# Optimization experiments

Measured on AMD Instinct MI355X. Metric: run time of the kernel, lower is better.

The kernel has to match this reference:

```python
import jax, jax.numpy as jnp
import numpy as np

B, S, D, H = 4, 2048, 256, 4
HD = D // H          # head_dim = 64
SPARSITY = 0.1
NH2 = H * H          # 16, distill feature size


def _linear_params(key, out_d, in_d):
    # torch nn.Linear default init: U(-1/sqrt(in), 1/sqrt(in)) for W and b
    limit = 1.0 / np.sqrt(in_d)
    kw, kb = jax.random.split(key)
    W = jax.random.uniform(kw, (out_d, in_d), minval=-limit, maxval=limit, dtype=jnp.float32)
    b = jax.random.uniform(kb, (out_d,), minval=-limit, maxval=limit, dtype=jnp.float32)
    return W, b


def setup_inputs() -> dict:
    key = jax.random.key(0)
    ks = jax.random.split(key, 8)
    x = jax.random.normal(ks[0], (B, S, D), dtype=jnp.float32)
    Wq, bq = _linear_params(ks[1], D, D)
    Wk, bk = _linear_params(ks[2], D, D)
    Wv, bv = _linear_params(ks[3], D, D)
    Wd, bd = _linear_params(ks[4], NH2, NH2)      # distill: 16 -> 16
    Wg, bg = _linear_params(ks[5], NH2, D)        # gate: dim -> 16 (then sigmoid)
    Wgp, bgp = _linear_params(ks[6], D, NH2)      # gate_projection: 16 -> dim
    Wo, bo = _linear_params(ks[7], D, D)          # out: dim -> dim
    return dict(x=x, Wq=Wq, bq=bq, Wk=Wk, bk=bk, Wv=Wv, bv=bv,
                Wd=Wd, bd=bd, Wg=Wg, bg=bg, Wgp=Wgp, bgp=bgp, Wo=Wo, bo=bo)


def reference(x, Wq, bq, Wk, bk, Wv, bv, Wd, bd, Wg, bg, Wgp, bgp, Wo, bo):
    b, s, d = x.shape
    scale = HD ** -0.5
    # QKV projections, split into heads: [b, h, s, hd]
    Q = (x @ Wq.T + bq).reshape(b, s, H, HD).transpose(0, 2, 1, 3)
    K = (x @ Wk.T + bk).reshape(b, s, H, HD).transpose(0, 2, 1, 3)
    V = (x @ Wv.T + bv).reshape(b, s, H, HD).transpose(0, 2, 1, 3)
    scores = jnp.einsum('bhqd,bhkd->bhqk', Q, K) * scale  # [b,h,s,s]
    # per-row quantile threshold (torch.quantile linear interpolation == jnp default)
    q = 1.0 - SPARSITY  # 0.9
    thr = jnp.quantile(scores, q, axis=-1, keepdims=True)
    masked = jnp.where(scores >= thr, scores, -jnp.inf)
    probs = jax.nn.softmax(masked, axis=-1)
    att = jnp.einsum('bhqk,bhkd->bhqd', probs, V)
    att = att.transpose(0, 2, 1, 3).reshape(b, s, d)  # [b,s,dim]
    # distill: view as (-1, 16) -> Linear(16,16) -> view back
    distilled = (att.reshape(-1, NH2) @ Wd.T + bd).reshape(b, s, d)
    # gate from mean-pooled input
    g = jax.nn.sigmoid(x.mean(axis=1) @ Wg.T + bg)  # [b,16]
    g = (g @ Wgp.T + bgp)[:, None, :]               # [b,1,dim] broadcast over seq
    mixed = g * distilled + (1.0 - g) * att
    return mixed @ Wo.T + bo
```

## Files before the change

kernel.cpp:

```cpp
#include <hip/hip_runtime.h>
#include <hip/hip_bf16.h>
#include <math.h>


#define CAP 256

typedef __attribute__((ext_vector_type(8))) short short8;
typedef __attribute__((ext_vector_type(4))) float floatx4;
typedef _Float16 half8 __attribute__((ext_vector_type(8)));
typedef _Float16 half4v __attribute__((ext_vector_type(4)));
#define MFMA16(a,b,c) __builtin_amdgcn_mfma_f32_16x16x32_bf16(a,b,c,0,0,0)
#define MFMAH(a,b,c)  __builtin_amdgcn_mfma_f32_16x16x32_f16(a,b,c,0,0,0)

__device__ __forceinline__ float umt(unsigned u){
  return __uint_as_float((u & 0x80000000u) ? (u & 0x7fffffffu) : ~u);
}
__device__ __forceinline__ float wsum_f(float v){
  #pragma unroll
  for (int m=1;m<64;m<<=1) v += __shfl_xor(v,m,64);
  return v;
}
__device__ __forceinline__ float wmax_f(float v){
  #pragma unroll
  for (int m=1;m<64;m<<=1) v = fmaxf(v, __shfl_xor(v,m,64));
  return v;
}
__device__ __forceinline__ float wmin_f(float v){
  #pragma unroll
  for (int m=1;m<64;m<<=1) v = fminf(v, __shfl_xor(v,m,64));
  return v;
}
__device__ __forceinline__ int mbcnt64(unsigned long long m){
  return (int)__builtin_amdgcn_mbcnt_hi((unsigned)(m>>32),
         __builtin_amdgcn_mbcnt_lo((unsigned)(m & 0xffffffffull), 0u));
}
__device__ __forceinline__ short8 ldb8(const __hip_bfloat16* p){
  return *(const short8*)p;
}

__global__ void xpart_kernel(const float* __restrict__ x, float* __restrict__ xpart){
  const int ch = blockIdx.x, b = blockIdx.y, t = threadIdx.x;
  const float* xp = x + ((size_t)b*2048 + (size_t)ch*128)*256 + t;
  float s = 0.f;
  for (int i=0;i<128;i++) s += xp[(size_t)i*256];
  xpart[(size_t)(b*16+ch)*256 + t] = s;
}

__global__ void gate_kernel(const float* __restrict__ xpart,
                            const float* __restrict__ Wg, const float* __restrict__ bg,
                            const float* __restrict__ Wgp,const float* __restrict__ bgp,
                            float* __restrict__ gate_ws){
  __shared__ float xm[256];
  __shared__ float g16[16];
  const int t = threadIdx.x;
  for (int b=0;b<4;b++){
    float s = 0.f;
    for (int ch=0; ch<16; ch++) s += xpart[(size_t)(b*16+ch)*256 + t];
    xm[t] = s * (1.0f/2048.0f);
    __syncthreads();
    if (t < 16){
      float z = bg[t];
      for (int d=0; d<256; d++) z = fmaf(xm[d], Wg[t*256+d], z);
      g16[t] = 1.0f/(1.0f + __expf(-z));
    }
    __syncthreads();
    float z2 = bgp[t];
    #pragma unroll
    for (int j=0;j<16;j++) z2 = fmaf(g16[j], Wgp[t*16+j], z2);
    gate_ws[b*256 + t] = z2;
    __syncthreads();
  }
}

__global__ __launch_bounds__(256) void qkv_gemm(
    const float* __restrict__ x,
    const float* __restrict__ Wq, const float* __restrict__ bq,
    const float* __restrict__ Wk, const float* __restrict__ bk,
    const float* __restrict__ Wv, const float* __restrict__ bv,
    __hip_bfloat16* __restrict__ qh, __hip_bfloat16* __restrict__ ql,
    __hip_bfloat16* __restrict__ kh, __hip_bfloat16* __restrict__ kl,
    _Float16* __restrict__ vth, _Float16* __restrict__ vtl){
  __shared__ float As[16][68];
  __shared__ float Bs[16][68];
  const int m0 = blockIdx.x * 64;
  const int n0g = blockIdx.y * 64;
  const int sect = n0g >> 8;
  const int nloc0 = n0g & 255;
  const float* W    = (sect==0) ? Wq : ((sect==1) ? Wk : Wv);
  const float* bias = (sect==0) ? bq : ((sect==1) ? bk : bv);
  const int tid = threadIdx.x;
  const int ty = tid >> 4, tx = tid & 15;
  const int lr = tid >> 2, lc = tid & 3;

  float c[4][4];
  #pragma unroll
  for (int i=0;i<4;i++){
    #pragma unroll
    for (int j=0;j<4;j++) c[i][j]=0.f;
  }

  for (int k0=0; k0<256; k0+=16){
    float4 av  = *(const float4*)&x[(size_t)(m0+lr)*256 + k0 + lc*4];
    float4 bv4 = *(const float4*)&W[(size_t)(nloc0+lr)*256 + k0 + lc*4];
    __syncthreads();
    As[lc*4+0][lr]=av.x;  As[lc*4+1][lr]=av.y;  As[lc*4+2][lr]=av.z;  As[lc*4+3][lr]=av.w;
    Bs[lc*4+0][lr]=bv4.x; Bs[lc*4+1][lr]=bv4.y; Bs[lc*4+2][lr]=bv4.z; Bs[lc*4+3][lr]=bv4.w;
    __syncthreads();
    #pragma unroll
    for (int kk=0; kk<16; kk++){
      float4 a  = *(const float4*)&As[kk][ty*4];
      float4 b4 = *(const float4*)&Bs[kk][tx*4];
      c[0][0]=fmaf(a.x,b4.x,c[0][0]); c[0][1]=fmaf(a.x,b4.y,c[0][1]); c[0][2]=fmaf(a.x,b4.z,c[0][2]); c[0][3]=fmaf(a.x,b4.w,c[0][3]);
      c[1][0]=fmaf(a.y,b4.x,c[1][0]); c[1][1]=fmaf(a.y,b4.y,c[1][1]); c[1][2]=fmaf(a.y,b4.z,c[1][2]); c[1][3]=fmaf(a.y,b4.w,c[1][3]);
      c[2][0]=fmaf(a.z,b4.x,c[2][0]); c[2][1]=fmaf(a.z,b4.y,c[2][1]); c[2][2]=fmaf(a.z,b4.z,c[2][2]); c[2][3]=fmaf(a.z,b4.w,c[2][3]);
      c[3][0]=fmaf(a.w,b4.x,c[3][0]); c[3][1]=fmaf(a.w,b4.y,c[3][1]); c[3][2]=fmaf(a.w,b4.z,c[3][2]); c[3][3]=fmaf(a.w,b4.w,c[3][3]);
    }
  }

  if (sect == 2){
    const int mB = m0 + ty*4;
    const int bidx = mB >> 11, s0 = mB & 2047;
    #pragma unroll
    for (int j=0;j<4;j++){
      const int f = nloc0 + tx*4 + j;
      const int hh = f >> 6, hd = f & 63;
      const float bf = bias[f];
      half4v hv, lv;
      #pragma unroll
      for (int i=0;i<4;i++){
        const float val = c[i][j] + bf;
        const _Float16 hx = (_Float16)val;
        hv[i] = hx;
        lv[i] = (_Float16)(val - (float)hx);
      }
      const size_t row = (size_t)((bidx*4+hh)*64 + hd);
      *(half4v*)(vth + row*2048 + s0) = hv;
      *(half4v*)(vtl + row*2048 + s0) = lv;
    }
  } else {
    #pragma unroll
    for (int i=0;i<4;i++){
      const int m = m0 + ty*4 + i;
      const int bidx = m >> 11, s = m & 2047;
      #pragma unroll
      for (int j=0;j<4;j++){
        const int f = nloc0 + tx*4 + j;
        const float val = c[i][j] + bias[f];
        const int hh = f >> 6, hd = f & 63;
        const size_t idx = (size_t)((bidx*4+hh)*2048 + s)*64 + hd;
        const __hip_bfloat16 hi = __float2bfloat16(val);
        const float lo = val - __bfloat162float(hi);
        if (sect == 0){ qh[idx] = hi; ql[idx] = __float2bfloat16(lo); }
        else          { kh[idx] = hi; kl[idx] = __float2bfloat16(lo); }
      }
    }
  }
}

__global__ __launch_bounds__(512, 4) void attn_kernel(
    const __hip_bfloat16* __restrict__ qh, const __hip_bfloat16* __restrict__ ql,
    const __hip_bfloat16* __restrict__ kh, const __hip_bfloat16* __restrict__ kl,
    const _Float16* __restrict__ vth, const _Float16* __restrict__ vtl,
    float* __restrict__ att_ws){
  __shared__ __align__(16) char smem[74240];
  __shared__ float obuf[16][66];
  __shared__ float zbuf[16];

  float (*buf0)[516] = (float (*)[516])smem;
  float (*buf1)[516] = (float (*)[516])(smem + 33024);

  const int bh = blockIdx.y;
  const int q0 = blockIdx.x * 16;
  const int tid = threadIdx.x;
  const int w = tid >> 6, ln = tid & 63;
  const int lm = ln & 15;
  const int lk = (ln >> 4) * 8;
  const int qa = 2*w, qb = 2*w + 1;

  const __hip_bfloat16* Qh = qh + ((size_t)bh*2048 + q0)*64;
  const __hip_bfloat16* Ql = ql + ((size_t)bh*2048 + q0)*64;
  const __hip_bfloat16* Kh = kh + ((size_t)bh*2048 + w*256)*64;
  const __hip_bfloat16* Kl = kl + ((size_t)bh*2048 + w*256)*64;

  float su0[32], su1[32];

  const short8 ah0 = ldb8(Qh + lm*64 + lk);
  const short8 ah1 = ldb8(Qh + lm*64 + 32 + lk);
  const short8 al0 = ldb8(Ql + lm*64 + lk);
  const short8 al1 = ldb8(Ql + lm*64 + 32 + lk);

  #pragma unroll
  for (int c = 0; c < 4; c++){
    float (*bufc)[516] = (c & 1) ? buf1 : buf0;
    floatx4 acc[4];
    #pragma unroll
    for (int tl = 0; tl < 4; tl++){
      const int krow = c*64 + tl*16 + lm;
      short8 bh0 = ldb8(Kh + krow*64 + lk);
      short8 bh1 = ldb8(Kh + krow*64 + 32 + lk);
      short8 bl0 = ldb8(Kl + krow*64 + lk);
      short8 bl1 = ldb8(Kl + krow*64 + 32 + lk);
      floatx4 a = {0.f,0.f,0.f,0.f};
      a = MFMA16(ah0, bh0, a);
      a = MFMA16(ah1, bh1, a);
      a = MFMA16(al0, bh0, a);
      a = MFMA16(al1, bh1, a);
      a = MFMA16(ah0, bl0, a);
      a = MFMA16(ah1, bl1, a);
      a = MFMA16(al0, bl0, a);
      a = MFMA16(al1, bl1, a);
      acc[tl] = a;
    }
    const int wr = (ln >> 4) * 4;
    #pragma unroll
    for (int tl = 0; tl < 4; tl++){
      const int col = w*64 + tl*16 + lm;
      bufc[wr+0][col] = acc[tl].x * 0.125f;
      bufc[wr+1][col] = acc[tl].y * 0.125f;
      bufc[wr+2][col] = acc[tl].z * 0.125f;
      bufc[wr+3][col] = acc[tl].w * 0.125f;
    }
    __syncthreads();
    float4 ra0 = *(const float4*)&bufc[qa][4*ln];
    float4 ra1 = *(const float4*)&bufc[qa][256 + 4*ln];
    float4 rb0 = *(const float4*)&bufc[qb][4*ln];
    float4 rb1 = *(const float4*)&bufc[qb][256 + 4*ln];
    const int o = c*8;
    su0[o+0]=ra0.x; su0[o+1]=ra0.y; su0[o+2]=ra0.z; su0[o+3]=ra0.w;
    su0[o+4]=ra1.x; su0[o+5]=ra1.y; su0[o+6]=ra1.z; su0[o+7]=ra1.w;
    su1[o+0]=rb0.x; su1[o+1]=rb0.y; su1[o+2]=rb0.z; su1[o+3]=rb0.w;
    su1[o+4]=rb1.x; su1[o+5]=rb1.y; su1[o+6]=rb1.z; su1[o+7]=rb1.w;
  }
  __syncthreads();

  unsigned p0 = 0, p1 = 0;
  #pragma unroll 1
  for (int bit = 31; bit >= 20; --bit){
    const float c0f = umt(p0 | (1u << bit));
    const float c1f = umt(p1 | (1u << bit));
    int n0 = 0, n1 = 0;
    #pragma unroll
    for (int i = 0; i < 32; i++){
      n0 += (int)__popcll(__ballot(su0[i] >= c0f));
      n1 += (int)__popcll(__ballot(su1[i] >= c1f));
    }
    if (n0 >= 206) p0 |= (1u << bit);
    if (n1 >= 206) p1 |= (1u << bit);
  }

  const int b = bh >> 2, h = bh & 3;

  #pragma unroll
  for (int rr = 0; rr < 2; rr++){
    const int q = 2*w + rr;
    const unsigned p = rr ? p1 : p0;
    const float pf  = umt(p);
    const float hif = umt(p + 0x100000u);
    float* candw = (float*)(smem + 66048 + (size_t)w*1024);

    int above = 0, nc = 0;
    float mx = -3.0e38f;
    #pragma unroll
    for (int i = 0; i < 32; i++){
      const float u = rr ? su1[i] : su0[i];
      mx = fmaxf(mx, u);
      const bool ab = (u >= hif);
      const bool cd = (u >= pf) && !ab;
      above += (int)__popcll(__ballot(ab));
      const unsigned long long bal = __ballot(cd);
      if (cd){
        const int pos = nc + mbcnt64(bal);
        if (pos < CAP) candw[pos] = u;
      }
      nc += (int)__popcll(bal);
    }
    mx = wmax_f(mx);

    unsigned v;
    if (nc <= CAP){
      const int j = 206 - above;
      const float cv0 = (ln       < nc) ? candw[ln]       : -3.0e38f;
      const float cv1 = (ln + 64  < nc) ? candw[ln + 64]  : -3.0e38f;
      const float cv2 = (ln + 128 < nc) ? candw[ln + 128] : -3.0e38f;
      const float cv3 = (ln + 192 < nc) ? candw[ln + 192] : -3.0e38f;
      v = p;
      #pragma unroll 1
      for (int bit = 19; bit >= 0; --bit){
        const float cf = umt(v | (1u << bit));
        int n = (int)__popcll(__ballot(cv0 >= cf))
              + (int)__popcll(__ballot(cv1 >= cf))
              + (int)__popcll(__ballot(cv2 >= cf))
              + (int)__popcll(__ballot(cv3 >= cf));
        if (n >= j) v |= (1u << bit);
      }
    } else {
      v = p;
      #pragma unroll 1
      for (int bit = 19; bit >= 0; --bit){
        const float cf = umt(v | (1u << bit));
        int n = 0;
        #pragma unroll
        for (int i = 0; i < 32; i++)
          n += (int)__popcll(__ballot((rr ? su1[i] : su0[i]) >= cf));
        if (n >= 206) v |= (1u << bit);
      }
    }
    const float v206 = umt(v);

    int cgt = 0; float mn = 3.0e38f;
    #pragma unroll
    for (int i = 0; i < 32; i++){
      const float u = rr ? su1[i] : su0[i];
      const bool gt = (u > v206);
      cgt += (int)__popcll(__ballot(gt));
      mn = (gt && u < mn) ? u : mn;
    }
    mn = wmin_f(mn);
    const float v205 = (cgt == 205) ? mn : v206;

    const float thr = (float)((double)v206 + 0.3*((double)v205 - (double)v206));

    float zl = 0.f;
    char* rowbase = smem + (size_t)q*4096 + ((size_t)(ln >> 4) << 9)
                  + (size_t)((((ln & 15) << 3)) ^ ((q & 7) << 4));
    #pragma unroll
    for (int c = 0; c < 4; c++){
      #pragma unroll
      for (int h4 = 0; h4 < 2; h4++){
        half4v pk;
        #pragma unroll
        for (int jj = 0; jj < 4; jj++){
          const int i = c*8 + h4*4 + jj;
          const float s = rr ? su1[i] : su0[i];
          const float pr = (s >= thr) ? __expf(s - mx) : 0.f;
          const _Float16 ph = (_Float16)pr;
          zl += (float)ph;
          pk[jj] = ph;
        }
        *(half4v*)(rowbase + h4*2048 + c*128) = pk;
      }
    }
    const float Z = wsum_f(zl);
    if (ln == 0) zbuf[q] = 1.0f / Z;
  }

  __syncthreads();

  const int ct = w & 3, kh2 = w >> 2;
  const int arow = ln & 15;
  const int sw = (arow & 7) << 4;
  const char* prow = smem + (size_t)arow*4096;
  const int klog0 = (kh2 << 11) + ((ln >> 4) << 4);
  const _Float16* vhp = vth + ((size_t)bh*64 + ct*16 + arow)*2048 + (kh2 << 10) + ((ln >> 4) << 3);
  const _Float16* vlp = vtl + ((size_t)bh*64 + ct*16 + arow)*2048 + (kh2 << 10) + ((ln >> 4) << 3);

  floatx4 acch = {0.f,0.f,0.f,0.f};
  floatx4 accl = {0.f,0.f,0.f,0.f};
  #pragma unroll 4
  for (int kk = 0; kk < 32; kk++){
    const half8 a   = *(const half8*)(prow + ((klog0 + kk*64) ^ sw));
    const half8 vh8 = *(const half8*)(vhp + kk*32);
    const half8 vl8 = *(const half8*)(vlp + kk*32);
    acch = MFMAH(a, vh8, acch);
    accl = MFMAH(a, vl8, accl);
  }
  floatx4 acc = acch + accl;

  if (kh2 == 1){
    const int r0 = (ln >> 4) * 4;
    #pragma unroll
    for (int i = 0; i < 4; i++) obuf[r0+i][ct*16 + arow] = acc[i];
  }
  __syncthreads();
  if (kh2 == 0){
    const int r0 = (ln >> 4) * 4;
    #pragma unroll
    for (int i = 0; i < 4; i++){
      const int r = r0 + i;
      const float o = (acc[i] + obuf[r][ct*16 + arow]) * zbuf[r];
      att_ws[(size_t)(b*2048 + q0 + r)*256 + h*64 + ct*16 + arow] = o;
    }
  }
}

__global__ void mix_kernel(const float* __restrict__ att,
                           const float* __restrict__ Wd, const float* __restrict__ bd,
                           const float* __restrict__ gate, float* __restrict__ mix){
  __shared__ float wd_s[256];
  __shared__ float bd_s[16];
  const int tid = threadIdx.x;
  wd_s[tid] = Wd[tid];
  if (tid < 16) bd_s[tid] = bd[tid];
  __syncthreads();
  const int m = blockIdx.x*16 + (tid >> 4);
  const int j = tid & 15;
  const int b = m >> 11;
  const float* arow = att + (size_t)m*256;
  float* mrow = mix + (size_t)m*256;
  for (int g=0; g<16; g++){
    float d = bd_s[j];
    #pragma unroll
    for (int mm=0; mm<16; mm++) d = fmaf(arow[g*16+mm], wd_s[j*16+mm], d);
    const int cidx = g*16 + j;
    const float gt = gate[b*256 + cidx];
    mrow[cidx] = gt*d + (1.0f - gt)*arow[cidx];
  }
}

__global__ __launch_bounds__(256) void out_gemm(
    const float* __restrict__ A, const float* __restrict__ Wo,
    const float* __restrict__ bo, float* __restrict__ out){
  __shared__ float As[16][68];
  __shared__ float Bs[16][68];
  const int m0 = blockIdx.x * 64;
  const int n0 = blockIdx.y * 64;
  const int tid = threadIdx.x;
  const int ty = tid >> 4, tx = tid & 15;
  const int lr = tid >> 2, lc = tid & 3;

  float c[4][4];
  #pragma unroll
  for (int i=0;i<4;i++){
    #pragma unroll
    for (int j=0;j<4;j++) c[i][j]=0.f;
  }

  for (int k0=0; k0<256; k0+=16){
    float4 av  = *(const float4*)&A[(size_t)(m0+lr)*256 + k0 + lc*4];
    float4 bv4 = *(const float4*)&Wo[(size_t)(n0+lr)*256 + k0 + lc*4];
    __syncthreads();
    As[lc*4+0][lr]=av.x;  As[lc*4+1][lr]=av.y;  As[lc*4+2][lr]=av.z;  As[lc*4+3][lr]=av.w;
    Bs[lc*4+0][lr]=bv4.x; Bs[lc*4+1][lr]=bv4.y; Bs[lc*4+2][lr]=bv4.z; Bs[lc*4+3][lr]=bv4.w;
    __syncthreads();
    #pragma unroll
    for (int kk=0; kk<16; kk++){
      float4 a  = *(const float4*)&As[kk][ty*4];
      float4 b4 = *(const float4*)&Bs[kk][tx*4];
      c[0][0]=fmaf(a.x,b4.x,c[0][0]); c[0][1]=fmaf(a.x,b4.y,c[0][1]); c[0][2]=fmaf(a.x,b4.z,c[0][2]); c[0][3]=fmaf(a.x,b4.w,c[0][3]);
      c[1][0]=fmaf(a.y,b4.x,c[1][0]); c[1][1]=fmaf(a.y,b4.y,c[1][1]); c[1][2]=fmaf(a.y,b4.z,c[1][2]); c[1][3]=fmaf(a.y,b4.w,c[1][3]);
      c[2][0]=fmaf(a.z,b4.x,c[2][0]); c[2][1]=fmaf(a.z,b4.y,c[2][1]); c[2][2]=fmaf(a.z,b4.z,c[2][2]); c[2][3]=fmaf(a.z,b4.w,c[2][3]);
      c[3][0]=fmaf(a.w,b4.x,c[3][0]); c[3][1]=fmaf(a.w,b4.y,c[3][1]); c[3][2]=fmaf(a.w,b4.z,c[3][2]); c[3][3]=fmaf(a.w,b4.w,c[3][3]);
    }
  }
  #pragma unroll
  for (int i=0;i<4;i++){
    const int m = m0 + ty*4 + i;
    float4 st = make_float4(c[i][0]+bo[n0+tx*4+0], c[i][1]+bo[n0+tx*4+1],
                            c[i][2]+bo[n0+tx*4+2], c[i][3]+bo[n0+tx*4+3]);
    *(float4*)&out[(size_t)m*256 + n0 + tx*4] = st;
  }
}

extern "C" void kernel_launch(void* const* d_in, const int* in_sizes, int n_in,
                              void* d_out, int out_size, void* d_ws, size_t ws_size,
                              hipStream_t stream) {
  const float* x   = (const float*)d_in[0];
  const float* Wq  = (const float*)d_in[1];  const float* bq  = (const float*)d_in[2];
  const float* Wk  = (const float*)d_in[3];  const float* bk  = (const float*)d_in[4];
  const float* Wv  = (const float*)d_in[5];  const float* bv  = (const float*)d_in[6];
  const float* Wd  = (const float*)d_in[7];  const float* bd  = (const float*)d_in[8];
  const float* Wg  = (const float*)d_in[9];  const float* bg  = (const float*)d_in[10];
  const float* Wgp = (const float*)d_in[11]; const float* bgp = (const float*)d_in[12];
  const float* Wo  = (const float*)d_in[13]; const float* bo  = (const float*)d_in[14];

  char* base = (char*)d_ws;
  float* att_ws = (float*)(base);
  float* mix_ws = (float*)(base + (size_t)( 8<<20));
  __hip_bfloat16* qh = (__hip_bfloat16*)(base + (size_t)(16<<20));
  __hip_bfloat16* ql = (__hip_bfloat16*)(base + (size_t)(20<<20));
  __hip_bfloat16* kh = (__hip_bfloat16*)(base + (size_t)(24<<20));
  __hip_bfloat16* kl = (__hip_bfloat16*)(base + (size_t)(28<<20));
  _Float16* vth = (_Float16*)(base + (size_t)(32<<20));
  _Float16* vtl = (_Float16*)(base + (size_t)(36<<20));
  float* xpart  = (float*)(base + (size_t)(40<<20));
  float* gate_ws= (float*)(base + (size_t)(40<<20) + 65536);

  xpart_kernel<<<dim3(16,4), 256, 0, stream>>>(x, xpart);
  gate_kernel<<<1, 256, 0, stream>>>(xpart, Wg, bg, Wgp, bgp, gate_ws);
  qkv_gemm<<<dim3(128,12), 256, 0, stream>>>(x, Wq,bq, Wk,bk, Wv,bv, qh,ql,kh,kl, vth,vtl);
  attn_kernel<<<dim3(128,16), 512, 0, stream>>>(qh, ql, kh, kl, vth, vtl, att_ws);
  mix_kernel<<<512, 256, 0, stream>>>(att_ws, Wd, bd, gate_ws, mix_ws);
  out_gemm<<<dim3(128,4), 256, 0, stream>>>(mix_ws, Wo, bo, (float*)d_out);
}
```

Measured before the change: 463.4 us.

## Fuse distill/gate mix into attention epilogue and parallelize gate kernel

Removes the separate mix kernel by computing the 16x16 distill projection and gate blend inside the attention epilogue, using wave shuffles across the 16 output columns. This drops a full fp32 att buffer round trip through global memory and one launch. The gate kernel now runs one block per batch instead of looping over batches. The 205th-order-statistic search uses the candidate registers and a tracked minimum of the above-threshold values, instead of rescanning all 32 score registers per row. The cost is more registers in the attention kernel for Wd and the gate values, which could lower occupancy.

```diff
diff --git a/kernel.cpp b/kernel.cpp
--- a/kernel.cpp
+++ b/kernel.cpp
@@ -53,23 +53,21 @@
   __shared__ float xm[256];
   __shared__ float g16[16];
   const int t = threadIdx.x;
-  for (int b=0;b<4;b++){
-    float s = 0.f;
-    for (int ch=0; ch<16; ch++) s += xpart[(size_t)(b*16+ch)*256 + t];
-    xm[t] = s * (1.0f/2048.0f);
-    __syncthreads();
-    if (t < 16){
-      float z = bg[t];
-      for (int d=0; d<256; d++) z = fmaf(xm[d], Wg[t*256+d], z);
-      g16[t] = 1.0f/(1.0f + __expf(-z));
-    }
-    __syncthreads();
-    float z2 = bgp[t];
-    #pragma unroll
-    for (int j=0;j<16;j++) z2 = fmaf(g16[j], Wgp[t*16+j], z2);
-    gate_ws[b*256 + t] = z2;
-    __syncthreads();
-  }
+  const int b = blockIdx.x;
+  float s = 0.f;
+  for (int ch=0; ch<16; ch++) s += xpart[(size_t)(b*16+ch)*256 + t];
+  xm[t] = s * (1.0f/2048.0f);
+  __syncthreads();
+  if (t < 16){
+    float z = bg[t];
+    for (int d=0; d<256; d++) z = fmaf(xm[d], Wg[t*256+d], z);
+    g16[t] = 1.0f/(1.0f + __expf(-z));
+  }
+  __syncthreads();
+  float z2 = bgp[t];
+  #pragma unroll
+  for (int j=0;j<16;j++) z2 = fmaf(g16[j], Wgp[t*16+j], z2);
+  gate_ws[b*256 + t] = z2;
 }
 
 __global__ __launch_bounds__(256) void qkv_gemm(
@@ -161,7 +159,8 @@
     const __hip_bfloat16* __restrict__ qh, const __hip_bfloat16* __restrict__ ql,
     const __hip_bfloat16* __restrict__ kh, const __hip_bfloat16* __restrict__ kl,
     const _Float16* __restrict__ vth, const _Float16* __restrict__ vtl,
-    float* __restrict__ att_ws){
+    const float* __restrict__ Wd, const float* __restrict__ bd,
+    const float* __restrict__ gate_ws, float* __restrict__ mix_ws){
   __shared__ __align__(16) char smem[74240];
   __shared__ float obuf[16][66];
   __shared__ float zbuf[16];
@@ -259,7 +258,7 @@
     float* candw = (float*)(smem + 66048 + (size_t)w*1024);
 
     int above = 0, nc = 0;
-    float mx = -3.0e38f;
+    float mx = -3.0e38f, mnab = 3.0e38f;
     #pragma unroll
     for (int i = 0; i < 32; i++){
       const float u = rr ? su1[i] : su0[i];
@@ -267,6 +266,7 @@
       const bool ab = (u >= hif);
       const bool cd = (u >= pf) && !ab;
       above += (int)__popcll(__ballot(ab));
+      if (ab) mnab = fminf(mnab, u);
       const unsigned long long bal = __ballot(cd);
       if (cd){
         const int pos = nc + mbcnt64(bal);
@@ -275,15 +275,16 @@
       nc += (int)__popcll(bal);
     }
     mx = wmax_f(mx);
-
-    unsigned v;
+    mnab = wmin_f(mnab);
+
+    float v206, v205;
     if (nc <= CAP){
       const int j = 206 - above;
       const float cv0 = (ln       < nc) ? candw[ln]       : -3.0e38f;
       const float cv1 = (ln + 64  < nc) ? candw[ln + 64]  : -3.0e38f;
       const float cv2 = (ln + 128 < nc) ? candw[ln + 128] : -3.0e38f;
       const float cv3 = (ln + 192 < nc) ? candw[ln + 192] : -3.0e38f;
-      v = p;
+      unsigned v = p;
       #pragma unroll 1
       for (int bit = 19; bit >= 0; --bit){
         const float cf = umt(v | (1u << bit));
@@ -293,8 +294,21 @@
               + (int)__popcll(__ballot(cv3 >= cf));
         if (n >= j) v |= (1u << bit);
       }
+      v206 = umt(v);
+      int cgtc = (int)__popcll(__ballot(cv0 > v206))
+               + (int)__popcll(__ballot(cv1 > v206))
+               + (int)__popcll(__ballot(cv2 > v206))
+               + (int)__popcll(__ballot(cv3 > v206));
+      float mnc = 3.0e38f;
+      if (cv0 > v206) mnc = fminf(mnc, cv0);
+      if (cv1 > v206) mnc = fminf(mnc, cv1);
+      if (cv2 > v206) mnc = fminf(mnc, cv2);
+      if (cv3 > v206) mnc = fminf(mnc, cv3);
+      mnc = wmin_f(mnc);
+      const int cgt = above + cgtc;
+      v205 = (cgt == 205) ? ((cgtc > 0) ? mnc : mnab) : v206;
     } else {
-      v = p;
+      unsigned v = p;
       #pragma unroll 1
       for (int bit = 19; bit >= 0; --bit){
         const float cf = umt(v | (1u << bit));
@@ -304,19 +318,18 @@
           n += (int)__popcll(__ballot((rr ? su1[i] : su0[i]) >= cf));
         if (n >= 206) v |= (1u << bit);
       }
-    }
-    const float v206 = umt(v);
-
-    int cgt = 0; float mn = 3.0e38f;
-    #pragma unroll
-    for (int i = 0; i < 32; i++){
-      const float u = rr ? su1[i] : su0[i];
-      const bool gt = (u > v206);
-      cgt += (int)__popcll(__ballot(gt));
-      mn = (gt && u < mn) ? u : mn;
-    }
-    mn = wmin_f(mn);
-    const float v205 = (cgt == 205) ? mn : v206;
+      v206 = umt(v);
+      int cgt = 0; float mn = 3.0e38f;
+      #pragma unroll
+      for (int i = 0; i < 32; i++){
+        const float u = rr ? su1[i] : su0[i];
+        const bool gt = (u > v206);
+        cgt += (int)__popcll(__ballot(gt));
+        mn = (gt && u < mn) ? u : mn;
+      }
+      mn = wmin_f(mn);
+      v205 = (cgt == 205) ? mn : v206;
+    }
 
     const float thr = (float)((double)v206 + 0.3*((double)v205 - (double)v206));
 
@@ -366,44 +379,36 @@
   }
   floatx4 acc = acch + accl;
 
+  float gt = 0.f, bda = 0.f;
+  float wdv[16];
   if (kh2 == 1){
     const int r0 = (ln >> 4) * 4;
     #pragma unroll
     for (int i = 0; i < 4; i++) obuf[r0+i][ct*16 + arow] = acc[i];
+  } else {
+    gt  = gate_ws[(size_t)b*256 + h*64 + ct*16 + arow];
+    bda = bd[arow];
+    #pragma unroll
+    for (int m4 = 0; m4 < 4; m4++){
+      const float4 t4 = *(const float4*)&Wd[arow*16 + m4*4];
+      wdv[m4*4+0]=t4.x; wdv[m4*4+1]=t4.y; wdv[m4*4+2]=t4.z; wdv[m4*4+3]=t4.w;
+    }
   }
   __syncthreads();
   if (kh2 == 0){
     const int r0 = (ln >> 4) * 4;
+    const int gb = ln & 48;
     #pragma unroll
     for (int i = 0; i < 4; i++){
       const int r = r0 + i;
       const float o = (acc[i] + obuf[r][ct*16 + arow]) * zbuf[r];
-      att_ws[(size_t)(b*2048 + q0 + r)*256 + h*64 + ct*16 + arow] = o;
-    }
-  }
-}
-
-__global__ void mix_kernel(const float* __restrict__ att,
-                           const float* __restrict__ Wd, const float* __restrict__ bd,
-                           const float* __restrict__ gate, float* __restrict__ mix){
-  __shared__ float wd_s[256];
-  __shared__ float bd_s[16];
-  const int tid = threadIdx.x;
-  wd_s[tid] = Wd[tid];
-  if (tid < 16) bd_s[tid] = bd[tid];
-  __syncthreads();
-  const int m = blockIdx.x*16 + (tid >> 4);
-  const int j = tid & 15;
-  const int b = m >> 11;
-  const float* arow = att + (size_t)m*256;
-  float* mrow = mix + (size_t)m*256;
-  for (int g=0; g<16; g++){
-    float d = bd_s[j];
-    #pragma unroll
-    for (int mm=0; mm<16; mm++) d = fmaf(arow[g*16+mm], wd_s[j*16+mm], d);
-    const int cidx = g*16 + j;
-    const float gt = gate[b*256 + cidx];
-    mrow[cidx] = gt*d + (1.0f - gt)*arow[cidx];
+      float d = bda;
+      #pragma unroll
+      for (int m = 0; m < 16; m++)
+        d = fmaf(__shfl(o, gb + m, 64), wdv[m], d);
+      const float mixed = gt*d + (1.0f - gt)*o;
+      mix_ws[(size_t)(b*2048 + q0 + r)*256 + h*64 + ct*16 + arow] = mixed;
+    }
   }
 }
 
@@ -464,21 +469,20 @@
   const float* Wo  = (const float*)d_in[13]; const float* bo  = (const float*)d_in[14];
 
   char* base = (char*)d_ws;
-  float* att_ws = (float*)(base);
-  float* mix_ws = (float*)(base + (size_t)( 8<<20));
-  __hip_bfloat16* qh = (__hip_bfloat16*)(base + (size_t)(16<<20));
-  __hip_bfloat16* ql = (__hip_bfloat16*)(base + (size_t)(20<<20));
-  __hip_bfloat16* kh = (__hip_bfloat16*)(base + (size_t)(24<<20));
-  __hip_bfloat16* kl = (__hip_bfloat16*)(base + (size_t)(28<<20));
-  _Float16* vth = (_Float16*)(base + (size_t)(32<<20));
-  _Float16* vtl = (_Float16*)(base + (size_t)(36<<20));
-  float* xpart  = (float*)(base + (size_t)(40<<20));
-  float* gate_ws= (float*)(base + (size_t)(40<<20) + 65536);
+  float* mix_ws = (float*)(base);
+  __hip_bfloat16* qh = (__hip_bfloat16*)(base + (size_t)( 8<<20));
+  __hip_bfloat16* ql = (__hip_bfloat16*)(base + (size_t)(12<<20));
+  __hip_bfloat16* kh = (__hip_bfloat16*)(base + (size_t)(16<<20));
+  __hip_bfloat16* kl = (__hip_bfloat16*)(base + (size_t)(20<<20));
+  _Float16* vth = (_Float16*)(base + (size_t)(24<<20));
+  _Float16* vtl = (_Float16*)(base + (size_t)(28<<20));
+  float* xpart  = (float*)(base + (size_t)(32<<20));
+  float* gate_ws= (float*)(base + (size_t)(32<<20) + 65536);
 
   xpart_kernel<<<dim3(16,4), 256, 0, stream>>>(x, xpart);
-  gate_kernel<<<1, 256, 0, stream>>>(xpart, Wg, bg, Wgp, bgp, gate_ws);
+  gate_kernel<<<4, 256, 0, stream>>>(xpart, Wg, bg, Wgp, bgp, gate_ws);
   qkv_gemm<<<dim3(128,12), 256, 0, stream>>>(x, Wq,bq, Wk,bk, Wv,bv, qh,ql,kh,kl, vth,vtl);
-  attn_kernel<<<dim3(128,16), 512, 0, stream>>>(qh, ql, kh, kl, vth, vtl, att_ws);
-  mix_kernel<<<512, 256, 0, stream>>>(att_ws, Wd, bd, gate_ws, mix_ws);
+  attn_kernel<<<dim3(128,16), 512, 0, stream>>>(qh, ql, kh, kl, vth, vtl,
+                                                Wd, bd, gate_ws, mix_ws);
   out_gemm<<<dim3(128,4), 256, 0, stream>>>(mix_ws, Wo, bo, (float*)d_out);
 }
```

Result: faster. 446.8 us (-3.6%).
